# Optimization experiments

Measured on AMD Instinct MI355X. Metric: run time of the kernel, lower is better.

Reference implementation:

```python
import jax, jax.numpy as jnp
import numpy as np

TAU = 0.1
EPS = 1e-8  # torch CosineSimilarity eps


def setup_inputs() -> dict:
    key = jax.random.key(0)
    k1, k2, k3 = jax.random.split(key, 3)
    B, D = 4096, 128
    z_i = jax.random.normal(k1, (B, D), dtype=jnp.float32)
    z_j = jax.random.normal(k2, (B, D), dtype=jnp.float32)
    y = jax.random.randint(k3, (B,), 0, 2)
    return {"z_i": z_i, "z_j": z_j, "y": y}


def reference(z_i, z_j, y):
    # p: (N, D) with N = 2B
    p = jnp.concatenate([z_i, z_j], axis=0)
    # cosine similarity via row-normalization + matmul (same math as the
    # broadcasted torch CosineSimilarity, without the O(N^2*D) intermediate)
    norm = jnp.maximum(jnp.linalg.norm(p, axis=1, keepdims=True), EPS)
    pn = p / norm
    sim = jnp.einsum('id,jd->ij', pn, pn) / TAU  # (N, N)

    N = sim.shape[0]
    y2 = jnp.concatenate([y, y], axis=0)
    eye = jnp.eye(N, dtype=sim.dtype)
    pos_mask = (y2[:, None] == y2[None, :]).astype(sim.dtype) * (1.0 - eye)
    logit_mask = 1.0 - eye

    # denominator excludes the diagonal (self-similarity)
    exp_logits = jnp.exp(sim) * logit_mask
    log_prob = sim - jnp.log(jnp.sum(exp_logits, axis=1, keepdims=True))
    mean_log_prob_pos = jnp.sum(pos_mask * log_prob, axis=1) / jnp.sum(pos_mask, axis=1)
    loss = -jnp.sum(mean_log_prob_pos)
    return loss
```

## Files before the change

kernel.cpp:

```cpp
#include <hip/hip_runtime.h>
#include <math.h>

#define BSZ 4096
#define NROW 8192
#define DIM 128
#define LOG2E10 14.426950408889634f

typedef __attribute__((ext_vector_type(8))) short bf16x8;
typedef __attribute__((ext_vector_type(4))) float f32x4;

#define PNH_F     (NROW * DIM / 2)
#define PNSWB_OFF PNH_F
#define PNSWA_OFF (2 * PNH_F)
#define G_OFF     (3 * PNH_F)
#define CNT_OFF   (G_OFF + 256)
#define SPART_OFF (G_OFF + 512)
#define PART_OFF  (SPART_OFF + 64 * NROW)

__device__ __forceinline__ unsigned short f2bf(float f) {
    unsigned u = __float_as_uint(f);
    return (unsigned short)((u + 0x7FFF + ((u >> 16) & 1)) >> 16);
}

__global__ void k_norm(const float* __restrict__ zi, const float* __restrict__ zj,
                       unsigned* __restrict__ pnh, unsigned* __restrict__ pnswB,
                       unsigned* __restrict__ pnswA, float* __restrict__ g) {
    int tid  = threadIdx.x;
    if (blockIdx.x == 0) g[tid] = 0.f;
    int wave = tid >> 6, lane = tid & 63;
    int row  = blockIdx.x * 4 + wave;
    const float* src = (row < BSZ) ? (zi + (size_t)row * DIM)
                                   : (zj + (size_t)(row - BSZ) * DIM);
    float2 v = ((const float2*)src)[lane];
    float ss = v.x * v.x + v.y * v.y;
    #pragma unroll
    for (int m = 32; m; m >>= 1) ss += __shfl_xor(ss, m, 64);
    float inv = 1.0f / fmaxf(sqrtf(ss), 1e-8f);
    float n0 = v.x * inv, n1 = v.y * inv;
    unsigned pack  = (unsigned)f2bf(n0) | ((unsigned)f2bf(n1) << 16);
    unsigned packA = (unsigned)f2bf(n0 * LOG2E10) | ((unsigned)f2bf(n1 * LOG2E10) << 16);
    pnh[(size_t)row * 64 + lane] = pack;
    int j = lane >> 2;
    int sw = ((j ^ (row & 15)) << 2) | (lane & 3);
    pnswB[(size_t)row * 64 + sw] = pack;
    pnswA[(size_t)row * 64 + sw] = packA;
}

__global__ void k_colsum(const unsigned* __restrict__ pnh, const int* __restrict__ y,
                         float* __restrict__ g, float* __restrict__ cnt) {
    __shared__ float red[4][4][64];
    int tid = threadIdx.x;
    if (blockIdx.x < 128) {
        int d2 = tid & 63;
        int rg = tid >> 6;
        int row0 = blockIdx.x * 64 + rg * 16;
        float s0a = 0.f, s0b = 0.f, s1a = 0.f, s1b = 0.f;
        #pragma unroll 4
        for (int i = 0; i < 16; ++i) {
            int r = row0 + i;
            unsigned u = pnh[(size_t)r * 64 + d2];
            float va = __uint_as_float(u << 16);
            float vb = __uint_as_float(u & 0xFFFF0000u);
            if (y[r & (BSZ - 1)]) { s1a += va; s1b += vb; }
            else                  { s0a += va; s0b += vb; }
        }
        red[rg][0][d2] = s0a; red[rg][1][d2] = s0b;
        red[rg][2][d2] = s1a; red[rg][3][d2] = s1b;
        __syncthreads();
        int lab = tid >> 7, d = tid & 127;
        int which = lab * 2 + (d & 1), dd2 = d >> 1;
        float s = red[0][which][dd2] + red[1][which][dd2]
                + red[2][which][dd2] + red[3][which][dd2];
        atomicAdd(&g[lab * DIM + d], s);
    } else {
        __shared__ float r0[256];
        float c = 0.f;
        for (int r = tid; r < BSZ; r += 256) c += (float)y[r];
        r0[tid] = c;
        __syncthreads();
        for (int s = 128; s; s >>= 1) {
            if (tid < s) r0[tid] += r0[tid + s];
            __syncthreads();
        }
        if (tid == 0) { cnt[1] = 2.0f * r0[0]; cnt[0] = (float)NROW - 2.0f * r0[0]; }
    }
}

__global__ __launch_bounds__(256, 4)
void k_expsum(const unsigned short* __restrict__ pnswA,
              const unsigned short* __restrict__ pnswB,
              float* __restrict__ spart) {
    int ti = blockIdx.y, tj = blockIdx.x;
    if (tj < ti) return;
    __shared__ short bt[128 * 128];
    __shared__ float rs_t[128];
    __shared__ float cs_p[4][128];
    int tid  = threadIdx.x;
    int lane = tid & 63;
    int w    = tid >> 6;
    int l15 = lane & 15, q = lane >> 4;
    bool isDiag = (ti == tj);
    int rwb = ti * 128 + w * 32;

    {
        const float4* src = (const float4*)(pnswB + (size_t)tj * 128 * DIM);
        float4* dst = (float4*)bt;
        #pragma unroll
        for (int i = 0; i < 8; ++i)
            dst[tid + 256 * i] = src[tid + 256 * i];
    }

    bf16x8 a[2][4];
    #pragma unroll
    for (int rf = 0; rf < 2; ++rf) {
        const unsigned short* ab = pnswA + (size_t)(rwb + rf * 16 + l15) * DIM;
        #pragma unroll
        for (int ks = 0; ks < 4; ++ks)
            a[rf][ks] = *(const bf16x8*)(ab + (((ks * 4 + q) ^ l15) << 3));
    }

    float rs[2][4], cs[8];
    #pragma unroll
    for (int rf = 0; rf < 2; ++rf)
        #pragma unroll
        for (int e = 0; e < 4; ++e) rs[rf][e] = 0.f;
    #pragma unroll
    for (int t = 0; t < 8; ++t) cs[t] = 0.f;

    __syncthreads();

    #pragma unroll
    for (int t = 0; t < 8; ++t) {
        bf16x8 b[4];
        #pragma unroll
        for (int ks = 0; ks < 4; ++ks)
            b[ks] = *(const bf16x8*)(bt + (t * 16 + l15) * 128 + (((ks * 4 + q) ^ l15) << 3));

        f32x4 acc[2];
        acc[0] = (f32x4){0.f, 0.f, 0.f, 0.f};
        acc[1] = (f32x4){0.f, 0.f, 0.f, 0.f};
        #pragma unroll
        for (int ks = 0; ks < 4; ++ks) {
            acc[0] = __builtin_amdgcn_mfma_f32_16x16x32_bf16(a[0][ks], b[ks], acc[0], 0, 0, 0);
            acc[1] = __builtin_amdgcn_mfma_f32_16x16x32_bf16(a[1][ks], b[ks], acc[1], 0, 0, 0);
        }

        if (isDiag && ((unsigned)(t * 16 - w * 32) < 32u)) {
            int col = tj * 128 + t * 16 + l15;
            #pragma unroll
            for (int rf = 0; rf < 2; ++rf)
                #pragma unroll
                for (int e = 0; e < 4; ++e) {
                    int row = rwb + rf * 16 + q * 4 + e;
                    float ex = exp2f(acc[rf][e]);
                    if (row == col) ex = 0.f;
                    rs[rf][e] += ex; cs[t] += ex;
                }
        } else {
            #pragma unroll
            for (int rf = 0; rf < 2; ++rf)
                #pragma unroll
                for (int e = 0; e < 4; ++e) {
                    float ex = exp2f(acc[rf][e]);
                    rs[rf][e] += ex; cs[t] += ex;
                }
        }
    }

    #pragma unroll
    for (int rf = 0; rf < 2; ++rf)
        #pragma unroll
        for (int e = 0; e < 4; ++e) {
            float v = rs[rf][e];
            v += __shfl_xor(v, 1, 16);
            v += __shfl_xor(v, 2, 16);
            v += __shfl_xor(v, 4, 16);
            v += __shfl_xor(v, 8, 16);
            if (l15 == 0) rs_t[w * 32 + rf * 16 + q * 4 + e] = v;
        }
    #pragma unroll
    for (int t = 0; t < 8; ++t) {
        float v = cs[t];
        v += __shfl_xor(v, 16, 64);
        v += __shfl_xor(v, 32, 64);
        if (q == 0) cs_p[w][t * 16 + l15] = v;
    }
    __syncthreads();

    if (tid < 128) {
        spart[(size_t)tj * NROW + ti * 128 + tid] = rs_t[tid];
    } else if (!isDiag) {
        int c = tid - 128;
        float v = cs_p[0][c] + cs_p[1][c] + cs_p[2][c] + cs_p[3][c];
        spart[(size_t)ti * NROW + tj * 128 + c] = v;
    }
}

__global__ void k_finalize(const unsigned* __restrict__ pnh, const float* __restrict__ spart,
                           const float* __restrict__ g, const float* __restrict__ cnt,
                           const int* __restrict__ y, float* __restrict__ partial) {
    __shared__ float red[4];
    int tid = threadIdx.x, wv = tid >> 6, lane = tid & 63;
    int row = blockIdx.x * 4 + wv;
    int lab = y[row & (BSZ - 1)];
    unsigned u = pnh[(size_t)row * 64 + lane];
    float p0 = __uint_as_float(u << 16);
    float p1 = __uint_as_float(u & 0xFFFF0000u);
    float2 gv = ((const float2*)(g + lab * DIM))[lane];
    float dg = p0 * gv.x + p1 * gv.y;
    float ds = p0 * p0 + p1 * p1;
    float sp = spart[(size_t)lane * NROW + row];
    #pragma unroll
    for (int m = 32; m; m >>= 1) {
        dg += __shfl_xor(dg, m, 64);
        ds += __shfl_xor(ds, m, 64);
        sp += __shfl_xor(sp, m, 64);
    }
    if (lane == 0) {
        float C = cnt[lab] - 1.0f;
        float P = (dg - ds) * 10.0f;
        red[wv] = logf(sp) - P / C;
    }
    __syncthreads();
    if (tid == 0) partial[blockIdx.x] = red[0] + red[1] + red[2] + red[3];
}

__global__ void k_sum(const float* __restrict__ partial, float* __restrict__ out) {
    __shared__ float red[256];
    float v = 0.f;
    #pragma unroll
    for (int i = 0; i < 8; ++i) v += partial[threadIdx.x + 256 * i];
    red[threadIdx.x] = v;
    __syncthreads();
    for (int s = 128; s; s >>= 1) {
        if (threadIdx.x < s) red[threadIdx.x] += red[threadIdx.x + s];
        __syncthreads();
    }
    if (threadIdx.x == 0) out[0] = red[0];
}

extern "C" void kernel_launch(void* const* d_in, const int* in_sizes, int n_in,
                              void* d_out, int out_size, void* d_ws, size_t ws_size,
                              hipStream_t stream) {
    const float* zi = (const float*)d_in[0];
    const float* zj = (const float*)d_in[1];
    const int*   y  = (const int*)d_in[2];
    float* out = (float*)d_out;
    float* ws  = (float*)d_ws;

    unsigned* pnh   = (unsigned*)ws;
    unsigned* pnswB = (unsigned*)(ws + PNSWB_OFF);
    unsigned* pnswA = (unsigned*)(ws + PNSWA_OFF);
    float* g       = ws + G_OFF;
    float* cnt     = ws + CNT_OFF;
    float* spart   = ws + SPART_OFF;
    float* partial = ws + PART_OFF;

    k_norm<<<NROW / 4, 256, 0, stream>>>(zi, zj, pnh, pnswB, pnswA, g);
    k_colsum<<<129, 256, 0, stream>>>(pnh, y, g, cnt);
    k_expsum<<<dim3(64, 64), 256, 0, stream>>>((const unsigned short*)pnswA,
                                               (const unsigned short*)pnswB, spart);
    k_finalize<<<NROW / 4, 256, 0, stream>>>(pnh, spart, g, cnt, y, partial);
    k_sum<<<1, 256, 0, stream>>>(partial, out);
}
```

Before: 100.7 us.

## Use a triangular grid, one shared scaled operand, and fuse the final sum

The exp-sum kernel now launches only the 2080 upper-triangular tile pairs, decoding (ti,tj) from a linear block index, instead of a 64x64 grid where half the blocks exit at once. The two bf16 copies (scaled A and plain B) are replaced by one copy scaled by sqrt(log2e/tau), so both operands share a buffer and k_norm writes less. The separate final reduction kernel is removed in favour of atomic accumulation plus a last-block counter in k_finalize. The trade-offs are a different bf16 rounding of the scaled product and float atomics whose summation order is not deterministic.

```diff
diff --git a/kernel.cpp b/kernel.cpp
--- a/kernel.cpp
+++ b/kernel.cpp
@@ -10,12 +10,10 @@
 typedef __attribute__((ext_vector_type(4))) float f32x4;
 
 #define PNH_F     (NROW * DIM / 2)
-#define PNSWB_OFF PNH_F
-#define PNSWA_OFF (2 * PNH_F)
-#define G_OFF     (3 * PNH_F)
+#define G_OFF     (2 * PNH_F)
 #define CNT_OFF   (G_OFF + 256)
+#define MISC_OFF  (CNT_OFF + 2)
 #define SPART_OFF (G_OFF + 512)
-#define PART_OFF  (SPART_OFF + 64 * NROW)
 
 __device__ __forceinline__ unsigned short f2bf(float f) {
     unsigned u = __float_as_uint(f);
@@ -23,10 +21,13 @@
 }
 
 __global__ void k_norm(const float* __restrict__ zi, const float* __restrict__ zj,
-                       unsigned* __restrict__ pnh, unsigned* __restrict__ pnswB,
-                       unsigned* __restrict__ pnswA, float* __restrict__ g) {
+                       unsigned* __restrict__ pnh, unsigned* __restrict__ pnsw,
+                       float* __restrict__ g, float* __restrict__ misc) {
     int tid  = threadIdx.x;
-    if (blockIdx.x == 0) g[tid] = 0.f;
+    if (blockIdx.x == 0) {
+        g[tid] = 0.f;
+        if (tid == 0) { misc[0] = 0.f; ((unsigned*)misc)[1] = 0u; }
+    }
     int wave = tid >> 6, lane = tid & 63;
     int row  = blockIdx.x * 4 + wave;
     const float* src = (row < BSZ) ? (zi + (size_t)row * DIM)
@@ -37,13 +38,12 @@
     for (int m = 32; m; m >>= 1) ss += __shfl_xor(ss, m, 64);
     float inv = 1.0f / fmaxf(sqrtf(ss), 1e-8f);
     float n0 = v.x * inv, n1 = v.y * inv;
-    unsigned pack  = (unsigned)f2bf(n0) | ((unsigned)f2bf(n1) << 16);
-    unsigned packA = (unsigned)f2bf(n0 * LOG2E10) | ((unsigned)f2bf(n1 * LOG2E10) << 16);
-    pnh[(size_t)row * 64 + lane] = pack;
+    pnh[(size_t)row * 64 + lane] = (unsigned)f2bf(n0) | ((unsigned)f2bf(n1) << 16);
+    const float s = sqrtf(LOG2E10);
+    unsigned packS = (unsigned)f2bf(n0 * s) | ((unsigned)f2bf(n1 * s) << 16);
     int j = lane >> 2;
     int sw = ((j ^ (row & 15)) << 2) | (lane & 3);
-    pnswB[(size_t)row * 64 + sw] = pack;
-    pnswA[(size_t)row * 64 + sw] = packA;
+    pnsw[(size_t)row * 64 + sw] = packS;
 }
 
 __global__ void k_colsum(const unsigned* __restrict__ pnh, const int* __restrict__ y,
@@ -87,11 +87,15 @@
 }
 
 __global__ __launch_bounds__(256, 4)
-void k_expsum(const unsigned short* __restrict__ pnswA,
-              const unsigned short* __restrict__ pnswB,
-              float* __restrict__ spart) {
-    int ti = blockIdx.y, tj = blockIdx.x;
-    if (tj < ti) return;
+void k_expsum(const unsigned short* __restrict__ pnsw, float* __restrict__ spart) {
+    int k = blockIdx.x;
+    float disc = sqrtf((float)(16641 - 8 * k));
+    int ti = (int)((129.0f - disc) * 0.5f);
+    int off = ti * (129 - ti) / 2;
+    if (off > k) { --ti; off = ti * (129 - ti) / 2; }
+    else { int off2 = (ti + 1) * (128 - ti) / 2; if (off2 <= k) { ti++; off = off2; } }
+    int tj = ti + (k - off);
+
     __shared__ short bt[128 * 128];
     __shared__ float rs_t[128];
     __shared__ float cs_p[4][128];
@@ -103,7 +107,7 @@
     int rwb = ti * 128 + w * 32;
 
     {
-        const float4* src = (const float4*)(pnswB + (size_t)tj * 128 * DIM);
+        const float4* src = (const float4*)(pnsw + (size_t)tj * 128 * DIM);
         float4* dst = (float4*)bt;
         #pragma unroll
         for (int i = 0; i < 8; ++i)
@@ -113,7 +117,7 @@
     bf16x8 a[2][4];
     #pragma unroll
     for (int rf = 0; rf < 2; ++rf) {
-        const unsigned short* ab = pnswA + (size_t)(rwb + rf * 16 + l15) * DIM;
+        const unsigned short* ab = pnsw + (size_t)(rwb + rf * 16 + l15) * DIM;
         #pragma unroll
         for (int ks = 0; ks < 4; ++ks)
             a[rf][ks] = *(const bf16x8*)(ab + (((ks * 4 + q) ^ l15) << 3));
@@ -198,7 +202,8 @@
 
 __global__ void k_finalize(const unsigned* __restrict__ pnh, const float* __restrict__ spart,
                            const float* __restrict__ g, const float* __restrict__ cnt,
-                           const int* __restrict__ y, float* __restrict__ partial) {
+                           const int* __restrict__ y, float* __restrict__ misc,
+                           float* __restrict__ out) {
     __shared__ float red[4];
     int tid = threadIdx.x, wv = tid >> 6, lane = tid & 63;
     int row = blockIdx.x * 4 + wv;
@@ -222,21 +227,16 @@
         red[wv] = logf(sp) - P / C;
     }
     __syncthreads();
-    if (tid == 0) partial[blockIdx.x] = red[0] + red[1] + red[2] + red[3];
-}
-
-__global__ void k_sum(const float* __restrict__ partial, float* __restrict__ out) {
-    __shared__ float red[256];
-    float v = 0.f;
-    #pragma unroll
-    for (int i = 0; i < 8; ++i) v += partial[threadIdx.x + 256 * i];
-    red[threadIdx.x] = v;
-    __syncthreads();
-    for (int s = 128; s; s >>= 1) {
-        if (threadIdx.x < s) red[threadIdx.x] += red[threadIdx.x + s];
-        __syncthreads();
-    }
-    if (threadIdx.x == 0) out[0] = red[0];
+    if (tid == 0) {
+        float v = red[0] + red[1] + red[2] + red[3];
+        atomicAdd(&misc[0], v);
+        __threadfence();
+        unsigned old = atomicAdd((unsigned*)&misc[1], 1u);
+        if (old == gridDim.x - 1) {
+            __threadfence();
+            out[0] = atomicAdd(&misc[0], 0.0f);
+        }
+    }
 }
 
 extern "C" void kernel_launch(void* const* d_in, const int* in_sizes, int n_in,
@@ -248,18 +248,15 @@
     float* out = (float*)d_out;
     float* ws  = (float*)d_ws;
 
-    unsigned* pnh   = (unsigned*)ws;
-    unsigned* pnswB = (unsigned*)(ws + PNSWB_OFF);
-    unsigned* pnswA = (unsigned*)(ws + PNSWA_OFF);
-    float* g       = ws + G_OFF;
-    float* cnt     = ws + CNT_OFF;
-    float* spart   = ws + SPART_OFF;
-    float* partial = ws + PART_OFF;
-
-    k_norm<<<NROW / 4, 256, 0, stream>>>(zi, zj, pnh, pnswB, pnswA, g);
+    unsigned* pnh  = (unsigned*)ws;
+    unsigned* pnsw = (unsigned*)(ws + PNH_F);
+    float* g     = ws + G_OFF;
+    float* cnt   = ws + CNT_OFF;
+    float* misc  = ws + MISC_OFF;
+    float* spart = ws + SPART_OFF;
+
+    k_norm<<<NROW / 4, 256, 0, stream>>>(zi, zj, pnh, pnsw, g, misc);
     k_colsum<<<129, 256, 0, stream>>>(pnh, y, g, cnt);
-    k_expsum<<<dim3(64, 64), 256, 0, stream>>>((const unsigned short*)pnswA,
-                                               (const unsigned short*)pnswB, spart);
-    k_finalize<<<NROW / 4, 256, 0, stream>>>(pnh, spart, g, cnt, y, partial);
-    k_sum<<<1, 256, 0, stream>>>(partial, out);
-}
+    k_expsum<<<2080, 256, 0, stream>>>((const unsigned short*)pnsw, spart);
+    k_finalize<<<NROW / 4, 256, 0, stream>>>(pnh, spart, g, cnt, y, misc, out);
+}
```

Result: slower. 207.6 us (+106.1%).
